# Kernel tuning notes

Hardware: AMD Instinct MI355X
Metric: run time of the kernel (lower is better)

## Reference

```python
import jax, jax.numpy as jnp
import numpy as np

B, INPUT_DIM, N = 8, 1, 4096
DIM, DEPTH, HEADS, DIM_HEAD = 512, 4, 8, 64
WINDOW = 128
NUM_CLASSES = 10
INNER = int(DIM * 4 * 2 / 3)  # 1365 (GEGLU FeedForward inner dim)
LN_EPS = 1e-5


def setup_inputs() -> dict:
    key = jax.random.key(0)
    ks = jax.random.split(key, 12)
    s = 0.02
    inner_qkv = HEADS * DIM_HEAD
    return {
        "x": jax.random.normal(ks[0], (B, INPUT_DIM, N), dtype=jnp.float32),
        "lin_emb_w": jax.random.normal(ks[1], (DIM, INPUT_DIM), dtype=jnp.float32) * s,
        "lin_emb_b": jnp.zeros((DIM,), dtype=jnp.float32),
        "qkv_w": jax.random.normal(ks[2], (DEPTH, 3 * inner_qkv, DIM), dtype=jnp.float32) * s,
        "out_w": jax.random.normal(ks[3], (DEPTH, DIM, inner_qkv), dtype=jnp.float32) * s,
        "ff_ln_g": jnp.ones((DEPTH, DIM), dtype=jnp.float32),
        "ff_ln_b": jnp.zeros((DEPTH, DIM), dtype=jnp.float32),
        "ff_w1": jax.random.normal(ks[4], (DEPTH, 2 * INNER, DIM), dtype=jnp.float32) * s,
        "ff_w2": jax.random.normal(ks[5], (DEPTH, DIM, INNER), dtype=jnp.float32) * s,
        "proj_w": jax.random.normal(ks[6], (NUM_CLASSES, DIM), dtype=jnp.float32) * s,
        "proj_b": jnp.zeros((NUM_CLASSES,), dtype=jnp.float32),
    }


def _layer_norm(x, g, b):
    mu = jnp.mean(x, axis=-1, keepdims=True)
    var = jnp.mean(jnp.square(x - mu), axis=-1, keepdims=True)
    return (x - mu) * jax.lax.rsqrt(var + LN_EPS) * g + b


def _local_attention(q, k, v, w):
    # q,k,v: (b, h, n, d). Non-causal sliding window: each window of size w
    # attends to windows [i-1, i, i+1] (look_backward=1, look_forward=1),
    # with out-of-range key positions masked (lucidrains LocalAttention,
    # autopad=True, exact_windowsize=False). n is a multiple of w here.
    b, h, n, d = q.shape
    nw = n // w
    scale = d ** -0.5
    qw = q.reshape(b, h, nw, w, d) * scale
    kw = k.reshape(b, h, nw, w, d)
    vw = v.reshape(b, h, nw, w, d)

    def look_around(t):  # (b,h,nw,w,d) -> (b,h,nw,3w,d)
        tp = jnp.pad(t, ((0, 0), (0, 0), (1, 1), (0, 0), (0, 0)))
        return jnp.concatenate([tp[:, :, i:i + nw] for i in range(3)], axis=3)

    k3 = look_around(kw)
    v3 = look_around(vw)

    # validity mask for boundary windows (fake keys from padding)
    win = jnp.arange(nw)
    kpos = (win[:, None] - 1) * w + jnp.arange(3 * w)[None, :]  # (nw, 3w)
    valid = (kpos >= 0) & (kpos < n)

    scores = jnp.einsum('bhnqd,bhnkd->bhnqk', qw, k3)  # (b,h,nw,w,3w)
    scores = jnp.where(valid[None, None, :, None, :], scores,
                       jnp.finfo(scores.dtype).min)
    attn = jax.nn.softmax(scores, axis=-1)
    out = jnp.einsum('bhnqk,bhnkd->bhnqd', attn, v3)
    return out.reshape(b, h, n, d)


def reference(x, lin_emb_w, lin_emb_b, qkv_w, out_w, ff_ln_g, ff_ln_b,
              ff_w1, ff_w2, proj_w, proj_b):
    b = x.shape[0]
    h = jnp.einsum('bdn,ed->bne', x, lin_emb_w) + lin_emb_b  # (b, n, dim)
    for l in range(DEPTH):
        # --- LocalMHA (no prenorm) + residual ---
        qkv = jnp.einsum('bnd,ed->bne', h, qkv_w[l])
        q, k, v = jnp.split(qkv, 3, axis=-1)
        def heads(t):
            return t.reshape(b, N, HEADS, DIM_HEAD).transpose(0, 2, 1, 3)
        o = _local_attention(heads(q), heads(k), heads(v), WINDOW)
        o = o.transpose(0, 2, 1, 3).reshape(b, N, HEADS * DIM_HEAD)
        h = jnp.einsum('bne,de->bnd', o, out_w[l]) + h
        # --- GEGLU FeedForward (prenorm inside) + residual ---
        y = _layer_norm(h, ff_ln_g[l], ff_ln_b[l])
        y = jnp.einsum('bnd,ed->bne', y, ff_w1[l])
        u, gate = jnp.split(y, 2, axis=-1)
        y = u * jax.nn.gelu(gate, approximate=False)
        h = h + jnp.einsum('bne,de->bnd', y, ff_w2[l])
    pooled = h.mean(axis=1)  # mean_pooling
    return pooled @ proj_w.T + proj_b
```

## Files before the change

### kernel.cpp

```cpp
#include <hip/hip_runtime.h>
#include <hip/hip_bf16.h>
#include <math.h>

typedef __attribute__((ext_vector_type(8))) short short8;
typedef __attribute__((ext_vector_type(4))) float f32x4;

#define MFMA16 __builtin_amdgcn_mfma_f32_16x16x32_bf16
#define GLOAD(dst, src) __builtin_amdgcn_global_load_lds( \
    (const __attribute__((address_space(1))) void*)(src), \
    (__attribute__((address_space(3))) void*)(dst), 16, 0, 0)

__device__ __forceinline__ short f2bf(float f){
  unsigned u = __float_as_uint(f);
  u = (u + 0x7FFFu + ((u >> 16) & 1u)) >> 16;
  return (short)u;
}

__device__ __forceinline__ size_t pidx(int r, int k, int K){
  return ((size_t)((r >> 8) * (K >> 5) + (k >> 5)) * 256 + (r & 255)) * 32 + (k & 31);
}

__device__ __forceinline__ float gelu_phi(float g){
  float ax = fabsf(g) * 0.70710678118f;
  float t  = 1.f / (1.f + 0.3275911f * ax);
  float pp = ((((1.061405429f * t - 1.453152027f) * t + 1.421413741f) * t
               - 0.284496736f) * t + 0.254829592f) * t;
  float e  = 1.f - pp * __expf(-ax * ax);
  return 0.5f + copysignf(0.5f, g) * e;
}

__global__ void cast_pack_kernel(const float* __restrict__ s, short* __restrict__ d,
                                 int NROW, int K){
  int i = blockIdx.x * 256 + threadIdx.x;
  int per = NROW * K;
  int l = i / per, rem = i - l * per;
  int r = rem / K, c = rem - r * K;
  d[(size_t)l * per + pidx(r, c, K)] = f2bf(s[i]);
}

__global__ void w1p_kernel(const float* __restrict__ s, short* __restrict__ d){
  int i = blockIdx.x * 256 + threadIdx.x;
  int c  = i & 511;
  int rl = i >> 9;
  int r  = rl % 2816;
  int l  = rl / 2816;
  int g  = r >> 5, sfx = r & 31;
  int j  = g * 16 + (sfx & 15);
  float v = 0.f;
  if (j < 1365){
    int sr = (sfx < 16) ? j : 1365 + j;
    v = s[((size_t)l * 2730 + sr) * 512 + c];
  }
  d[(size_t)l * 2816 * 512 + pidx(r, c, 512)] = f2bf(v);
}

__global__ void w2p_kernel(const float* __restrict__ s, short* __restrict__ d){
  int i = blockIdx.x * 256 + threadIdx.x;
  int c = i % 1408;
  int rr = i / 1408;
  int l = rr >> 9, row = rr & 511;
  float v = (c < 1365) ? s[(size_t)rr * 1365 + c] : 0.f;
  d[(size_t)l * 512 * 1408 + pidx(row, c, 1408)] = f2bf(v);
}

__global__ void embed_kernel(const float* __restrict__ x, const float* __restrict__ w,
                             const float* __restrict__ bias, float* __restrict__ hf,
                             short* __restrict__ hb){
  long i = ((long)blockIdx.x * 256 + threadIdx.x) * 8;
  long row = i >> 9; int e = (int)(i & 511);
  float xv = x[row];
  float4 w0 = *(const float4*)(w + e),    w1 = *(const float4*)(w + e + 4);
  float4 b0 = *(const float4*)(bias + e), b1 = *(const float4*)(bias + e + 4);
  float4 o0, o1;
  o0.x = xv*w0.x+b0.x; o0.y = xv*w0.y+b0.y; o0.z = xv*w0.z+b0.z; o0.w = xv*w0.w+b0.w;
  o1.x = xv*w1.x+b1.x; o1.y = xv*w1.y+b1.y; o1.z = xv*w1.z+b1.z; o1.w = xv*w1.w+b1.w;
  *(float4*)(hf + i) = o0; *(float4*)(hf + i + 4) = o1;
  short8 hv;
  hv[0]=f2bf(o0.x); hv[1]=f2bf(o0.y); hv[2]=f2bf(o0.z); hv[3]=f2bf(o0.w);
  hv[4]=f2bf(o1.x); hv[5]=f2bf(o1.y); hv[6]=f2bf(o1.z); hv[7]=f2bf(o1.w);
  *(short8*)(hb + pidx((int)row, e, 512)) = hv;
}

template<int EPI>
__global__ __launch_bounds__(1024, 4)
void gemm_pk(const short* __restrict__ A, const short* __restrict__ B, int K,
             float* __restrict__ Cres, short* __restrict__ Cbf, int ldcb)
{
  __shared__ short As[4][256][32];
  __shared__ short Bs[4][256][32];
  char* smA = (char*)As; char* smB = (char*)Bs;
  const int tid = threadIdx.x, lane = tid & 63, w = tid >> 6;
  const int wm = w >> 2, wn = w & 3;
  const int NT = K >> 5;
  const int nwg = gridDim.x * gridDim.y;
  const int f = blockIdx.y * gridDim.x + blockIdx.x;
  const int sw = (f & 7) * (nwg >> 3) + (f >> 3);
  const long tm = (long)(sw / gridDim.x) * 256;
  const long tn = (long)(sw % gridDim.x) * 256;

  const int srow = tid >> 2;
  const int sc   = (tid & 3) ^ ((srow >> 1) & 3);
  const short* aS = A + ((size_t)(tm >> 8) * NT * 256 + srow) * 32 + sc * 8;
  const short* bS = B + ((size_t)(tn >> 8) * NT * 256 + srow) * 32 + sc * 8;
  const int ldsW = w * 1024;

  f32x4 acc[4][4];
  #pragma unroll
  for (int i = 0; i < 4; i++)
    #pragma unroll
    for (int j = 0; j < 4; j++) acc[i][j] = (f32x4){0.f,0.f,0.f,0.f};

  const int rA = wm * 64 + (lane & 15);
  const int rB = wn * 64 + (lane & 15);
  const int abase = rA * 64 + (((lane >> 4) ^ ((rA >> 1) & 3)) * 16);
  const int bbase = rB * 64 + (((lane >> 4) ^ ((rB >> 1) & 3)) * 16);

  GLOAD(smA + 0 + ldsW, aS);             GLOAD(smB + 0 + ldsW, bS);
  GLOAD(smA + 16384 + ldsW, aS + 8192);  GLOAD(smB + 16384 + ldsW, bS + 8192);
  GLOAD(smA + 32768 + ldsW, aS + 16384); GLOAD(smB + 32768 + ldsW, bS + 16384);
  asm volatile("s_waitcnt vmcnt(4)" ::: "memory");
  __builtin_amdgcn_s_barrier();

  for (int t = 0; t < NT; ++t){
    const int cur = (t & 3) * 16384;
    const int stb = ((t + 3) & 3) * 16384;
    const size_t ko = (size_t)(t + 3) * 8192;
    if (t + 3 < NT){ GLOAD(smA + stb + ldsW, aS + ko); GLOAD(smB + stb + ldsW, bS + ko); }
    short8 a[4], bb[4];
    #pragma unroll
    for (int ni = 0; ni < 4; ni++)
      bb[ni] = *(const short8*)(smB + cur + bbase + ni * 1024);
    #pragma unroll
    for (int q = 0; q < 4; q++)
      a[q] = *(const short8*)(smA + cur + abase + q * 1024);
    #pragma unroll
    for (int q = 0; q < 4; q++)
      #pragma unroll
      for (int ni = 0; ni < 4; ni++)
        acc[q][ni] = MFMA16(a[q], bb[ni], acc[q][ni], 0, 0, 0);
    if      (t + 3 < NT) asm volatile("s_waitcnt vmcnt(4)" ::: "memory");
    else if (t + 2 < NT) asm volatile("s_waitcnt vmcnt(2)" ::: "memory");
    else if (t + 1 < NT) asm volatile("s_waitcnt vmcnt(0)" ::: "memory");
    __builtin_amdgcn_s_barrier();
  }

  #pragma unroll
  for (int mi = 0; mi < 4; mi++){
    if (EPI == 3){
      #pragma unroll
      for (int p = 0; p < 2; p++)
        #pragma unroll
        for (int v = 0; v < 4; v++){
          int row = (int)(tm + wm * 64 + mi * 16 + (lane >> 4) * 4 + v);
          int col = (int)((tn >> 1) + wn * 32 + p * 16 + (lane & 15));
          float u = acc[mi][2*p][v], g = acc[mi][2*p+1][v];
          Cbf[pidx(row, col, 1408)] = f2bf(u * g * gelu_phi(g));
        }
    } else {
      #pragma unroll
      for (int ni = 0; ni < 4; ni++)
        #pragma unroll
        for (int v = 0; v < 4; v++){
          int row = (int)(tm + wm * 64 + mi * 16 + (lane >> 4) * 4 + v);
          int col = (int)(tn + wn * 64 + ni * 16 + (lane & 15));
          float x = acc[mi][ni][v];
          if (EPI == 4){
            int hd = col >> 6, d = col & 63;
            Cbf[((size_t)hd * 32768 + row) * 64 + d] = f2bf(x);
          } else if (EPI == 1){
            Cres[(long)row * 512 + col] = x + Cres[(long)row * 512 + col];
          } else {
            float rr = x + Cres[(long)row * 512 + col];
            Cres[(long)row * 512 + col] = rr;
            Cbf[pidx(row, col, 512)] = f2bf(rr);
          }
        }
    }
  }
}

__global__ __launch_bounds__(256, 2)
void attn_kernel(const short* __restrict__ qkv, short* __restrict__ o)
{
  __shared__ short Ks[128 * 64];
  __shared__ short Vt[64 * 136];
  __shared__ short Ps[4 * 32 * 128];
  char* smK = (char*)Ks;
  const int win = blockIdx.x, hh = blockIdx.y, b = blockIdx.z;
  const int tid = threadIdx.x, lane = tid & 63, w = tid >> 6;
  const long qrow0 = (long)b * 4096 + (long)win * 128;
  const short* Qb = qkv + (size_t)hh * 2097152;
  const short* Kb = qkv + (size_t)(8 + hh) * 2097152;
  const short* Vb = qkv + (size_t)(16 + hh) * 2097152;

  short8 qf[2][2];
  #pragma unroll
  for (int i = 0; i < 2; i++)
    #pragma unroll
    for (int kk = 0; kk < 2; kk++)
      qf[i][kk] = *(const short8*)(Qb + (qrow0 + w * 32 + i * 16 + (lane & 15)) * 64
                                   + kk * 32 + (lane >> 4) * 8);

  f32x4 oacc[2][4];
  #pragma unroll
  for (int i = 0; i < 2; i++)
    #pragma unroll
    for (int j = 0; j < 4; j++) oacc[i][j] = (f32x4){0.f,0.f,0.f,0.f};
  float rs[2][4];
  #pragma unroll
  for (int i = 0; i < 2; i++)
    #pragma unroll
    for (int v = 0; v < 4; v++) rs[i][v] = 0.f;

  const int row_s = tid >> 3;
  const int c_s   = tid & 7;
  const int schK  = (tid & 7) ^ ((tid >> 3) & 7);
  for (int cc = 0; cc < 3; cc++){
    int kw = win - 1 + cc;
    if (kw < 0 || kw >= 32) continue;
    const long krow0 = (long)b * 4096 + (long)kw * 128;
    __syncthreads();
    const short* srcK = Kb + (krow0 + row_s) * 64 + schK * 8;
    const short* srcV = Vb + (krow0 + row_s) * 64 + c_s * 8;
    #pragma unroll
    for (int r = 0; r < 4; r++){
      GLOAD(smK + w * 1024 + r * 4096, srcK + (size_t)r * 32 * 64);
      short8 vv = *(const short8*)(srcV + (size_t)r * 32 * 64);
      int row = row_s + r * 32;
      #pragma unroll
      for (int e = 0; e < 8; e++) Vt[(c_s * 8 + e) * 136 + row] = vv[e];
    }
    __syncthreads();

    f32x4 sacc[2][8];
    #pragma unroll
    for (int i = 0; i < 2; i++)
      #pragma unroll
      for (int j = 0; j < 8; j++) sacc[i][j] = (f32x4){0.f,0.f,0.f,0.f};
    #pragma unroll
    for (int kk = 0; kk < 2; kk++){
      short8 bbk[8];
      int ac = (kk * 32 + (lane >> 4) * 8) * 2;
      #pragma unroll
      for (int j = 0; j < 8; j++){
        int br = j * 16 + (lane & 15);
        bbk[j] = *(const short8*)((char*)Ks + ((br * 128 + ac) ^ ((br & 7) << 4)));
      }
      #pragma unroll
      for (int i = 0; i < 2; i++)
        #pragma unroll
        for (int j = 0; j < 8; j++)
          sacc[i][j] = MFMA16(qf[i][kk], bbk[j], sacc[i][j], 0, 0, 0);
    }

    short* myPs = Ps + w * 32 * 128;
    float psum[2][4];
    #pragma unroll
    for (int i = 0; i < 2; i++)
      #pragma unroll
      for (int v = 0; v < 4; v++) psum[i][v] = 0.f;
    #pragma unroll
    for (int i = 0; i < 2; i++)
      #pragma unroll
      for (int j = 0; j < 8; j++)
        #pragma unroll
        for (int v = 0; v < 4; v++){
          float p = __expf(0.125f * sacc[i][j][v]);
          psum[i][v] += p;
          int prow = i * 16 + (lane >> 4) * 4 + v;
          int pcb  = (j * 16 + (lane & 15)) * 2;
          *(short*)((char*)myPs + ((prow * 256 + pcb) ^ ((prow & 7) << 4))) = f2bf(p);
        }
    #pragma unroll
    for (int i = 0; i < 2; i++)
      #pragma unroll
      for (int v = 0; v < 4; v++){
        float s = psum[i][v];
        s += __shfl_xor(s, 1); s += __shfl_xor(s, 2);
        s += __shfl_xor(s, 4); s += __shfl_xor(s, 8);
        rs[i][v] += s;
      }
    __syncthreads();

    #pragma unroll
    for (int kk = 0; kk < 4; kk++){
      short8 pa[2], vb[4];
      int kb = (kk * 32 + (lane >> 4) * 8) * 2;
      #pragma unroll
      for (int i = 0; i < 2; i++){
        int pr = i * 16 + (lane & 15);
        pa[i] = *(const short8*)((char*)myPs + ((pr * 256 + kb) ^ ((pr & 7) << 4)));
      }
      #pragma unroll
      for (int j = 0; j < 4; j++){
        int vr = j * 16 + (lane & 15);
        vb[j] = *(const short8*)((char*)Vt + (vr * 272 + kb));
      }
      #pragma unroll
      for (int i = 0; i < 2; i++)
        #pragma unroll
        for (int j = 0; j < 4; j++)
          oacc[i][j] = MFMA16(pa[i], vb[j], oacc[i][j], 0, 0, 0);
    }
  }

  #pragma unroll
  for (int i = 0; i < 2; i++)
    #pragma unroll
    for (int j = 0; j < 4; j++)
      #pragma unroll
      for (int v = 0; v < 4; v++){
        int row = (int)(qrow0 + w * 32 + i * 16 + (lane >> 4) * 4 + v);
        int col = hh * 64 + j * 16 + (lane & 15);
        o[pidx(row, col, 512)] = f2bf(oacc[i][j][v] / rs[i][v]);
      }
}

__global__ __launch_bounds__(256)
void ln_kernel(const float* __restrict__ h, const float* __restrict__ g,
               const float* __restrict__ be, short* __restrict__ y)
{
  long row = (long)blockIdx.x * 4 + (threadIdx.x >> 6);
  int lane = threadIdx.x & 63;
  const float* x = h + row * 512 + lane * 8;
  float4 a0 = *(const float4*)x;
  float4 a1 = *(const float4*)(x + 4);
  float v[8] = {a0.x, a0.y, a0.z, a0.w, a1.x, a1.y, a1.z, a1.w};
  float s = 0.f, sq = 0.f;
  #pragma unroll
  for (int j = 0; j < 8; j++){ s += v[j]; sq += v[j] * v[j]; }
  #pragma unroll
  for (int m = 1; m <= 32; m <<= 1){ s += __shfl_xor(s, m); sq += __shfl_xor(sq, m); }
  float mu = s * (1.f / 512.f);
  float var = sq * (1.f / 512.f) - mu * mu;
  float rstd = rsqrtf(var + 1e-5f);
  short8 yv;
  #pragma unroll
  for (int j = 0; j < 8; j++){
    int c = lane * 8 + j;
    yv[j] = f2bf((v[j] - mu) * rstd * g[c] + be[c]);
  }
  *(short8*)(y + pidx((int)row, lane * 8, 512)) = yv;
}

__global__ void pool_partial(const float* __restrict__ h, float* __restrict__ part){
  int b = blockIdx.x, ch = blockIdx.y, t = threadIdx.x;
  float s0 = 0.f, s1 = 0.f;
  const float* base = h + ((long)b * 4096 + ch * 128) * 512;
  for (int n = 0; n < 128; n++){
    s0 += base[(long)n * 512 + t];
    s1 += base[(long)n * 512 + t + 256];
  }
  part[((b * 32 + ch) * 512) + t] = s0;
  part[((b * 32 + ch) * 512) + t + 256] = s1;
}

__global__ void pool_proj(const float* __restrict__ part, const float* __restrict__ pw,
                          const float* __restrict__ pb, float* __restrict__ out){
  __shared__ float pooled[512];
  __shared__ float red[4];
  int b = blockIdx.x, t = threadIdx.x;
  int lane = t & 63, w = t >> 6;
  float s0 = 0.f, s1 = 0.f;
  for (int ch = 0; ch < 32; ch++){
    s0 += part[((b * 32 + ch) * 512) + t];
    s1 += part[((b * 32 + ch) * 512) + t + 256];
  }
  pooled[t] = s0 * (1.f / 4096.f);
  pooled[t + 256] = s1 * (1.f / 4096.f);
  __syncthreads();
  for (int cls = 0; cls < 10; cls++){
    float p = pooled[t] * pw[cls * 512 + t] + pooled[t + 256] * pw[cls * 512 + t + 256];
    p += __shfl_xor(p, 1); p += __shfl_xor(p, 2); p += __shfl_xor(p, 4);
    p += __shfl_xor(p, 8); p += __shfl_xor(p, 16); p += __shfl_xor(p, 32);
    if (lane == 0) red[w] = p;
    __syncthreads();
    if (t == 0) out[b * 10 + cls] = red[0] + red[1] + red[2] + red[3] + pb[cls];
    __syncthreads();
  }
}

extern "C" void kernel_launch(void* const* d_in, const int* in_sizes, int n_in,
                              void* d_out, int out_size, void* d_ws, size_t ws_size,
                              hipStream_t stream)
{
  const float* x      = (const float*)d_in[0];
  const float* lin_w  = (const float*)d_in[1];
  const float* lin_b  = (const float*)d_in[2];
  const float* qkvw_f = (const float*)d_in[3];
  const float* outw_f = (const float*)d_in[4];
  const float* lng    = (const float*)d_in[5];
  const float* lnb    = (const float*)d_in[6];
  const float* w1_f   = (const float*)d_in[7];
  const float* w2_f   = (const float*)d_in[8];
  const float* projw  = (const float*)d_in[9];
  const float* projb  = (const float*)d_in[10];
  float* out = (float*)d_out;

  char* ws = (char*)d_ws;
  float* hf32 = (float*)(ws);
  short* abuf = (short*)(ws + 67108864);
  short* qkvb = (short*)(ws + 100663296);
  short* gbuf = qkvb;
  short* obuf = (short*)(ws + 201326592);
  float* part = (float*)(ws + 234881024);
  short* wqkv = (short*)(ws + 235405312);
  short* wout = (short*)(ws + 247988224);
  short* w1p  = (short*)(ws + 250085376);
  short* w2p  = (short*)(ws + 261619712);

  cast_pack_kernel<<<12288, 256, 0, stream>>>(qkvw_f, wqkv, 1536, 512);
  cast_pack_kernel<<<4096, 256, 0, stream>>>(outw_f, wout, 512, 512);
  w1p_kernel<<<22528, 256, 0, stream>>>(w1_f, w1p);
  w2p_kernel<<<11264, 256, 0, stream>>>(w2_f, w2p);
  embed_kernel<<<8192, 256, 0, stream>>>(x, lin_w, lin_b, hf32, abuf);

  for (int l = 0; l < 4; l++){
    gemm_pk<4><<<dim3(6, 128), 1024, 0, stream>>>(abuf, wqkv + (size_t)l * 1536 * 512, 512,
                                                  nullptr, qkvb, 0);
    attn_kernel<<<dim3(32, 8, 8), 256, 0, stream>>>(qkvb, obuf);
    gemm_pk<1><<<dim3(2, 128), 1024, 0, stream>>>(obuf, wout + (size_t)l * 512 * 512, 512,
                                                  hf32, nullptr, 0);
    ln_kernel<<<8192, 256, 0, stream>>>(hf32, lng + l * 512, lnb + l * 512, abuf);
    gemm_pk<3><<<dim3(11, 128), 1024, 0, stream>>>(abuf, w1p + (size_t)l * 2816 * 512, 512,
                                                   nullptr, gbuf, 1408);
    gemm_pk<2><<<dim3(2, 128), 1024, 0, stream>>>(gbuf, w2p + (size_t)l * 512 * 1408, 1408,
                                                  hf32, abuf, 512);
  }
  pool_partial<<<dim3(8, 32), 256, 0, stream>>>(hf32, part);
  pool_proj<<<8, 256, 0, stream>>>(part, projw, projb, out);
}
```

Baseline: 1.803 ms.

## Load GEMM B operand directly into double-buffered registers, bypassing LDS

In the packed bf16 GEMM, the B tile is no longer staged through shared memory. Each wave now reads its B fragments straight from global memory into two register buffers, prefetching one k-step ahead, while A keeps its 4-stage LDS pipeline. The aim is to halve LDS footprint and LDS read traffic, and to drop the B stores into shared memory. The cost is that the four waves sharing a column block each fetch the same B data from global/L2, which multiplies that traffic. The fixed vmcnt(6) wait at the pipeline tail may also not cover the final A tiles, which risks a race.

Result: slower. 1.976 ms (+9.6%).

```diff
diff --git a/kernel.cpp b/kernel.cpp
--- a/kernel.cpp
+++ b/kernel.cpp
@@ -87,8 +87,7 @@
              float* __restrict__ Cres, short* __restrict__ Cbf, int ldcb)
 {
   __shared__ short As[4][256][32];
-  __shared__ short Bs[4][256][32];
-  char* smA = (char*)As; char* smB = (char*)Bs;
+  char* smA = (char*)As;
   const int tid = threadIdx.x, lane = tid & 63, w = tid >> 6;
   const int wm = w >> 2, wn = w & 3;
   const int NT = K >> 5;
@@ -101,9 +100,11 @@
   const int srow = tid >> 2;
   const int sc   = (tid & 3) ^ ((srow >> 1) & 3);
   const short* aS = A + ((size_t)(tm >> 8) * NT * 256 + srow) * 32 + sc * 8;
-  const short* bS = B + ((size_t)(tn >> 8) * NT * 256 + srow) * 32 + sc * 8;
   const int ldsW = w * 1024;
 
+  const short* bF = B + (size_t)(tn >> 8) * NT * 8192
+                      + (size_t)(wn * 64 + (lane & 15)) * 32 + (lane >> 4) * 8;
+
   f32x4 acc[4][4];
   #pragma unroll
   for (int i = 0; i < 4; i++)
@@ -111,38 +112,46 @@
     for (int j = 0; j < 4; j++) acc[i][j] = (f32x4){0.f,0.f,0.f,0.f};
 
   const int rA = wm * 64 + (lane & 15);
-  const int rB = wn * 64 + (lane & 15);
   const int abase = rA * 64 + (((lane >> 4) ^ ((rA >> 1) & 3)) * 16);
-  const int bbase = rB * 64 + (((lane >> 4) ^ ((rB >> 1) & 3)) * 16);
-
-  GLOAD(smA + 0 + ldsW, aS);             GLOAD(smB + 0 + ldsW, bS);
-  GLOAD(smA + 16384 + ldsW, aS + 8192);  GLOAD(smB + 16384 + ldsW, bS + 8192);
-  GLOAD(smA + 32768 + ldsW, aS + 16384); GLOAD(smB + 32768 + ldsW, bS + 16384);
-  asm volatile("s_waitcnt vmcnt(4)" ::: "memory");
+
+  short8 bX[4], bY[4];
+
+  GLOAD(smA + 0 + ldsW, aS);
+  #pragma unroll
+  for (int ni = 0; ni < 4; ni++) bX[ni] = *(const short8*)(bF + ni * 512);
+  GLOAD(smA + 16384 + ldsW, aS + 8192);
+  GLOAD(smA + 32768 + ldsW, aS + 16384);
+  asm volatile("s_waitcnt vmcnt(2)" ::: "memory");
   __builtin_amdgcn_s_barrier();
 
-  for (int t = 0; t < NT; ++t){
-    const int cur = (t & 3) * 16384;
-    const int stb = ((t + 3) & 3) * 16384;
-    const size_t ko = (size_t)(t + 3) * 8192;
-    if (t + 3 < NT){ GLOAD(smA + stb + ldsW, aS + ko); GLOAD(smB + stb + ldsW, bS + ko); }
-    short8 a[4], bb[4];
-    #pragma unroll
-    for (int ni = 0; ni < 4; ni++)
-      bb[ni] = *(const short8*)(smB + cur + bbase + ni * 1024);
-    #pragma unroll
-    for (int q = 0; q < 4; q++)
-      a[q] = *(const short8*)(smA + cur + abase + q * 1024);
-    #pragma unroll
-    for (int q = 0; q < 4; q++)
-      #pragma unroll
-      for (int ni = 0; ni < 4; ni++)
-        acc[q][ni] = MFMA16(a[q], bb[ni], acc[q][ni], 0, 0, 0);
-    if      (t + 3 < NT) asm volatile("s_waitcnt vmcnt(4)" ::: "memory");
-    else if (t + 2 < NT) asm volatile("s_waitcnt vmcnt(2)" ::: "memory");
-    else if (t + 1 < NT) asm volatile("s_waitcnt vmcnt(0)" ::: "memory");
-    __builtin_amdgcn_s_barrier();
-  }
+  #define TILE_BODY(T, BU, BL)                                              \
+  {                                                                          \
+    const int cur = ((T) & 3) * 16384;                                       \
+    if ((T) + 1 < NT){                                                       \
+      _Pragma("unroll")                                                      \
+      for (int ni = 0; ni < 4; ni++)                                         \
+        BL[ni] = *(const short8*)(bF + (size_t)((T) + 1) * 8192 + ni * 512); \
+    }                                                                        \
+    if ((T) + 3 < NT)                                                        \
+      GLOAD(smA + (((T) + 3) & 3) * 16384 + ldsW, aS + (size_t)((T) + 3) * 8192); \
+    short8 a_[4];                                                            \
+    _Pragma("unroll")                                                        \
+    for (int q = 0; q < 4; q++)                                              \
+      a_[q] = *(const short8*)(smA + cur + abase + q * 1024);                \
+    _Pragma("unroll")                                                        \
+    for (int q = 0; q < 4; q++)                                              \
+      _Pragma("unroll")                                                      \
+      for (int ni = 0; ni < 4; ni++)                                         \
+        acc[q][ni] = MFMA16(a_[q], BU[ni], acc[q][ni], 0, 0, 0);             \
+    asm volatile("s_waitcnt vmcnt(6)" ::: "memory");                         \
+    __builtin_amdgcn_s_barrier();                                            \
+  }
+
+  for (int t = 0; t < NT; t += 2){
+    TILE_BODY(t,     bX, bY)
+    TILE_BODY(t + 1, bY, bX)
+  }
+  #undef TILE_BODY
 
   #pragma unroll
   for (int mi = 0; mi < 4; mi++){
```

## Alias attention P buffer onto K shared memory to raise occupancy

Applied to the files above, without the earlier changes.

Drops the separate per-wave probability buffer and reuses the K tile's shared memory for P once the QK^T products are done. Softmax and PV run in two 64-column halves so each wave's P slice fits in 4 KB of the K region. This cuts LDS use enough to request three blocks per CU instead of two, aiming to hide latency better. In exchange it adds a barrier and splits the work into two phases, which serialises some work.

Result: slower. 2.171 ms (+20.4%).

```diff
diff --git a/kernel.cpp b/kernel.cpp
--- a/kernel.cpp
+++ b/kernel.cpp
@@ -179,13 +179,12 @@
   }
 }
 
-__global__ __launch_bounds__(256, 2)
+__global__ __launch_bounds__(256, 3)
 void attn_kernel(const short* __restrict__ qkv, short* __restrict__ o)
 {
-  __shared__ short Ks[128 * 64];
+  __shared__ short KP[128 * 64];
   __shared__ short Vt[64 * 136];
-  __shared__ short Ps[4 * 32 * 128];
-  char* smK = (char*)Ks;
+  char* smK = (char*)KP;
   const int win = blockIdx.x, hh = blockIdx.y, b = blockIdx.z;
   const int tid = threadIdx.x, lane = tid & 63, w = tid >> 6;
   const long qrow0 = (long)b * 4096 + (long)win * 128;
@@ -215,6 +214,8 @@
   const int row_s = tid >> 3;
   const int c_s   = tid & 7;
   const int schK  = (tid & 7) ^ ((tid >> 3) & 7);
+  char* myPs = (char*)KP + w * 4096;
+
   for (int cc = 0; cc < 3; cc++){
     int kw = win - 1 + cc;
     if (kw < 0 || kw >= 32) continue;
@@ -239,38 +240,98 @@
       for (int j = 0; j < 8; j++) sacc[i][j] = (f32x4){0.f,0.f,0.f,0.f};
     #pragma unroll
     for (int kk = 0; kk < 2; kk++){
-      short8 bbk[8];
       int ac = (kk * 32 + (lane >> 4) * 8) * 2;
       #pragma unroll
-      for (int j = 0; j < 8; j++){
-        int br = j * 16 + (lane & 15);
-        bbk[j] = *(const short8*)((char*)Ks + ((br * 128 + ac) ^ ((br & 7) << 4)));
-      }
-      #pragma unroll
-      for (int i = 0; i < 2; i++)
-        #pragma unroll
-        for (int j = 0; j < 8; j++)
-          sacc[i][j] = MFMA16(qf[i][kk], bbk[j], sacc[i][j], 0, 0, 0);
+      for (int jh = 0; jh < 2; jh++){
+        short8 bbk[4];
+        #pragma unroll
+        for (int jj = 0; jj < 4; jj++){
+          int br = (jh * 4 + jj) * 16 + (lane & 15);
+          bbk[jj] = *(const short8*)(smK + ((br * 128 + ac) ^ ((br & 7) << 4)));
+        }
+        #pragma unroll
+        for (int i = 0; i < 2; i++)
+          #pragma unroll
+          for (int jj = 0; jj < 4; jj++)
+            sacc[i][jh * 4 + jj] = MFMA16(qf[i][kk], bbk[jj], sacc[i][jh * 4 + jj], 0, 0, 0);
+      }
     }
-
-    short* myPs = Ps + w * 32 * 128;
+    __syncthreads();
+
     float psum[2][4];
     #pragma unroll
     for (int i = 0; i < 2; i++)
       #pragma unroll
       for (int v = 0; v < 4; v++) psum[i][v] = 0.f;
+
     #pragma unroll
     for (int i = 0; i < 2; i++)
       #pragma unroll
-      for (int j = 0; j < 8; j++)
+      for (int j = 0; j < 4; j++)
         #pragma unroll
         for (int v = 0; v < 4; v++){
           float p = __expf(0.125f * sacc[i][j][v]);
           psum[i][v] += p;
           int prow = i * 16 + (lane >> 4) * 4 + v;
           int pcb  = (j * 16 + (lane & 15)) * 2;
-          *(short*)((char*)myPs + ((prow * 256 + pcb) ^ ((prow & 7) << 4))) = f2bf(p);
+          *(short*)(myPs + ((prow * 128 + pcb) ^ ((prow & 7) << 4))) = f2bf(p);
         }
+    #pragma unroll
+    for (int kk = 0; kk < 2; kk++){
+      short8 pa[2], vb[4];
+      int kb = (kk * 32 + (lane >> 4) * 8) * 2;
+      #pragma unroll
+      for (int i = 0; i < 2; i++){
+        int pr = i * 16 + (lane & 15);
+        pa[i] = *(const short8*)(myPs + ((pr * 128 + kb) ^ ((pr & 7) << 4)));
+      }
+      #pragma unroll
+      for (int j = 0; j < 4; j++){
+        int vr = j * 16 + (lane & 15);
+        vb[j] = *(const short8*)((char*)Vt + (vr * 272 + kb));
+      }
+      #pragma unroll
+      for (int i = 0; i < 2; i++)
+        #pragma unroll
+        for (int j = 0; j < 4; j++)
+          oacc[i][j] = MFMA16(pa[i], vb[j], oacc[i][j], 0, 0, 0);
+    }
+    asm volatile("s_waitcnt lgkmcnt(0)" ::: "memory");
+
+    #pragma unroll
+    for (int i = 0; i < 2; i++)
+      #pragma unroll
+      for (int j = 4; j < 8; j++)
+        #pragma unroll
+        for (int v = 0; v < 4; v++){
+          float p = __expf(0.125f * sacc[i][j][v]);
+          psum[i][v] += p;
+          int prow = i * 16 + (lane >> 4) * 4 + v;
+          int pcb  = ((j - 4) * 16 + (lane & 15)) * 2;
+          *(short*)(myPs + ((prow * 128 + pcb) ^ ((prow & 7) << 4))) = f2bf(p);
+        }
+    #pragma unroll
+    for (int kk = 2; kk < 4; kk++){
+      short8 pa[2], vb[4];
+      int kbL = ((kk - 2) * 32 + (lane >> 4) * 8) * 2;
+      int kbV = (kk * 32 + (lane >> 4) * 8) * 2;
+      #pragma unroll
+      for (int i = 0; i < 2; i++){
+        int pr = i * 16 + (lane & 15);
+        pa[i] = *(const short8*)(myPs + ((pr * 128 + kbL) ^ ((pr & 7) << 4)));
+      }
+      #pragma unroll
+      for (int j = 0; j < 4; j++){
+        int vr = j * 16 + (lane & 15);
+        vb[j] = *(const short8*)((char*)Vt + (vr * 272 + kbV));
+      }
+      #pragma unroll
+      for (int i = 0; i < 2; i++)
+        #pragma unroll
+        for (int j = 0; j < 4; j++)
+          oacc[i][j] = MFMA16(pa[i], vb[j], oacc[i][j], 0, 0, 0);
+    }
+
     #pragma unroll
     for (int i = 0; i < 2; i++)
       #pragma unroll
@@ -280,28 +341,6 @@
         s += __shfl_xor(s, 4); s += __shfl_xor(s, 8);
         rs[i][v] += s;
       }
-    __syncthreads();
-
-    #pragma unroll
-    for (int kk = 0; kk < 4; kk++){
-      short8 pa[2], vb[4];
-      int kb = (kk * 32 + (lane >> 4) * 8) * 2;
-      #pragma unroll
-      for (int i = 0; i < 2; i++){
-        int pr = i * 16 + (lane & 15);
-        pa[i] = *(const short8*)((char*)myPs + ((pr * 256 + kb) ^ ((pr & 7) << 4)));
-      }
-      #pragma unroll
-      for (int j = 0; j < 4; j++){
-        int vr = j * 16 + (lane & 15);
-        vb[j] = *(const short8*)((char*)Vt + (vr * 272 + kb));
-      }
-      #pragma unroll
-      for (int i = 0; i < 2; i++)
-        #pragma unroll
-        for (int j = 0; j < 4; j++)
-          oacc[i][j] = MFMA16(pa[i], vb[j], oacc[i][j], 0, 0, 0);
-    }
   }
 
   #pragma unroll
```

## Process two query windows per attention block to share K/V tile loads

Applied to the files above, without the earlier changes.

Each attention block now computes two adjacent 128-row query windows, loading four K/V windows once and reusing the middle two for both. The per-window load of K and the transposed V into shared memory is cut from three to two on average. Blocks are also remapped from a 1D grid so neighbouring (batch, head) work is grouped, likely for cache locality across dies. The cost is doubled accumulator registers, possible occupancy loss, and half as many blocks.

After: 2.265 ms. 1.26x slower.

```diff
diff --git a/kernel.cpp b/kernel.cpp
--- a/kernel.cpp
+++ b/kernel.cpp
@@ -186,52 +186,47 @@
   __shared__ short Vt[64 * 136];
   __shared__ short Ps[4 * 32 * 128];
   char* smK = (char*)Ks;
-  const int win = blockIdx.x, hh = blockIdx.y, b = blockIdx.z;
+  const int fdec = (blockIdx.x & 7) * 128 + (blockIdx.x >> 3);
+  const int wp = fdec & 15, hh = (fdec >> 4) & 7, b = fdec >> 7;
+  const int winA = wp * 2;
   const int tid = threadIdx.x, lane = tid & 63, w = tid >> 6;
-  const long qrow0 = (long)b * 4096 + (long)win * 128;
+  const long qrowA = (long)b * 4096 + (long)winA * 128;
+  const long qrowB = qrowA + 128;
   const short* Qb = qkv + (size_t)hh * 2097152;
   const short* Kb = qkv + (size_t)(8 + hh) * 2097152;
   const short* Vb = qkv + (size_t)(16 + hh) * 2097152;
 
-  short8 qf[2][2];
+  short8 qfA[2][2], qfB[2][2];
   #pragma unroll
   for (int i = 0; i < 2; i++)
     #pragma unroll
-    for (int kk = 0; kk < 2; kk++)
-      qf[i][kk] = *(const short8*)(Qb + (qrow0 + w * 32 + i * 16 + (lane & 15)) * 64
-                                   + kk * 32 + (lane >> 4) * 8);
-
-  f32x4 oacc[2][4];
+    for (int kk = 0; kk < 2; kk++){
+      qfA[i][kk] = *(const short8*)(Qb + (qrowA + w * 32 + i * 16 + (lane & 15)) * 64
+                                    + kk * 32 + (lane >> 4) * 8);
+      qfB[i][kk] = *(const short8*)(Qb + (qrowB + w * 32 + i * 16 + (lane & 15)) * 64
+                                    + kk * 32 + (lane >> 4) * 8);
+    }
+
+  f32x4 oaccA[2][4], oaccB[2][4];
+  float rsA[2][4], rsB[2][4];
   #pragma unroll
   for (int i = 0; i < 2; i++)
     #pragma unroll
-    for (int j = 0; j < 4; j++) oacc[i][j] = (f32x4){0.f,0.f,0.f,0.f};
-  float rs[2][4];
+    for (int j = 0; j < 4; j++){
+      oaccA[i][j] = (f32x4){0.f,0.f,0.f,0.f};
+      oaccB[i][j] = (f32x4){0.f,0.f,0.f,0.f};
+    }
   #pragma unroll
   for (int i = 0; i < 2; i++)
     #pragma unroll
-    for (int v = 0; v < 4; v++) rs[i][v] = 0.f;
+    for (int v = 0; v < 4; v++){ rsA[i][v] = 0.f; rsB[i][v] = 0.f; }
 
   const int row_s = tid >> 3;
   const int c_s   = tid & 7;
   const int schK  = (tid & 7) ^ ((tid >> 3) & 7);
-  for (int cc = 0; cc < 3; cc++){
-    int kw = win - 1 + cc;
-    if (kw < 0 || kw >= 32) continue;
-    const long krow0 = (long)b * 4096 + (long)kw * 128;
-    __syncthreads();
-    const short* srcK = Kb + (krow0 + row_s) * 64 + schK * 8;
-    const short* srcV = Vb + (krow0 + row_s) * 64 + c_s * 8;
-    #pragma unroll
-    for (int r = 0; r < 4; r++){
-      GLOAD(smK + w * 1024 + r * 4096, srcK + (size_t)r * 32 * 64);
-      short8 vv = *(const short8*)(srcV + (size_t)r * 32 * 64);
-      int row = row_s + r * 32;
-      #pragma unroll
-      for (int e = 0; e < 8; e++) Vt[(c_s * 8 + e) * 136 + row] = vv[e];
-    }
-    __syncthreads();
-
+  short* myPs = Ps + w * 32 * 128;
+
+  auto PASS = [&](short8 (&qf)[2][2], f32x4 (&oacc)[2][4], float (&rs)[2][4]){
     f32x4 sacc[2][8];
     #pragma unroll
     for (int i = 0; i < 2; i++)
@@ -239,21 +234,22 @@
       for (int j = 0; j < 8; j++) sacc[i][j] = (f32x4){0.f,0.f,0.f,0.f};
     #pragma unroll
     for (int kk = 0; kk < 2; kk++){
-      short8 bbk[8];
       int ac = (kk * 32 + (lane >> 4) * 8) * 2;
       #pragma unroll
-      for (int j = 0; j < 8; j++){
-        int br = j * 16 + (lane & 15);
-        bbk[j] = *(const short8*)((char*)Ks + ((br * 128 + ac) ^ ((br & 7) << 4)));
+      for (int jh = 0; jh < 2; jh++){
+        short8 bbk[4];
+        #pragma unroll
+        for (int jj = 0; jj < 4; jj++){
+          int br = (jh * 4 + jj) * 16 + (lane & 15);
+          bbk[jj] = *(const short8*)(smK + ((br * 128 + ac) ^ ((br & 7) << 4)));
+        }
+        #pragma unroll
+        for (int i = 0; i < 2; i++)
+          #pragma unroll
+          for (int jj = 0; jj < 4; jj++)
+            sacc[i][jh * 4 + jj] = MFMA16(qf[i][kk], bbk[jj], sacc[i][jh * 4 + jj], 0, 0, 0);
       }
-      #pragma unroll
-      for (int i = 0; i < 2; i++)
-        #pragma unroll
-        for (int j = 0; j < 8; j++)
-          sacc[i][j] = MFMA16(qf[i][kk], bbk[j], sacc[i][j], 0, 0, 0);
-    }
-
-    short* myPs = Ps + w * 32 * 128;
+    }
     float psum[2][4];
     #pragma unroll
     for (int i = 0; i < 2; i++)
@@ -281,7 +277,6 @@
         rs[i][v] += s;
       }
     __syncthreads();
-
     #pragma unroll
     for (int kk = 0; kk < 4; kk++){
       short8 pa[2], vb[4];
@@ -302,6 +297,30 @@
         for (int j = 0; j < 4; j++)
           oacc[i][j] = MFMA16(pa[i], vb[j], oacc[i][j], 0, 0, 0);
     }
+  };
+
+  for (int cc = 0; cc < 4; cc++){
+    int kw = winA - 1 + cc;
+    if (kw < 0 || kw >= 32) continue;
+    const long krow0 = (long)b * 4096 + (long)kw * 128;
+    __syncthreads();
+    const short* srcK = Kb + (krow0 + row_s) * 64 + schK * 8;
+    const short* srcV = Vb + (krow0 + row_s) * 64 + c_s * 8;
+    #pragma unroll
+    for (int r = 0; r < 4; r++){
+      GLOAD(smK + w * 1024 + r * 4096, srcK + (size_t)r * 32 * 64);
+      short8 vv = *(const short8*)(srcV + (size_t)r * 32 * 64);
+      int row = row_s + r * 32;
+      #pragma unroll
+      for (int e = 0; e < 8; e++) Vt[(c_s * 8 + e) * 136 + row] = vv[e];
+    }
+    __syncthreads();
+
+    if (cc < 3) PASS(qfA, oaccA, rsA);
+    if (cc > 0){
+      asm volatile("s_waitcnt lgkmcnt(0)" ::: "memory");
+      PASS(qfB, oaccB, rsB);
+    }
   }
 
   #pragma unroll
@@ -310,9 +329,10 @@
     for (int j = 0; j < 4; j++)
       #pragma unroll
       for (int v = 0; v < 4; v++){
-        int row = (int)(qrow0 + w * 32 + i * 16 + (lane >> 4) * 4 + v);
+        int rowA = (int)(qrowA + w * 32 + i * 16 + (lane >> 4) * 4 + v);
         int col = hh * 64 + j * 16 + (lane & 15);
-        o[pidx(row, col, 512)] = f2bf(oacc[i][j][v] / rs[i][v]);
+        o[pidx(rowA, col, 512)] = f2bf(oaccA[i][j][v] / rsA[i][v]);
+        o[pidx(rowA + 128, col, 512)] = f2bf(oaccB[i][j][v] / rsB[i][v]);
       }
 }
 
@@ -418,7 +438,7 @@
   for (int l = 0; l < 4; l++){
     gemm_pk<4><<<dim3(6, 128), 1024, 0, stream>>>(abuf, wqkv + (size_t)l * 1536 * 512, 512,
                                                   nullptr, qkvb, 0);
-    attn_kernel<<<dim3(32, 8, 8), 256, 0, stream>>>(qkvb, obuf);
+    attn_kernel<<<1024, 256, 0, stream>>>(qkvb, obuf);
     gemm_pk<1><<<dim3(2, 128), 1024, 0, stream>>>(obuf, wout + (size_t)l * 512 * 512, 512,
                                                   hf32, nullptr, 0);
     ln_kernel<<<8192, 256, 0, stream>>>(hf32, lng + l * 512, lnb + l * 512, abuf);
```
